# Performance work log

Measured on AMD Instinct MI355X. Metric: run time of the kernel, lower is better.

Reference implementation:

```python
import jax, jax.numpy as jnp
import numpy as np

COMMITMENT_COST = 0.25


def setup_inputs() -> dict:
    key = jax.random.key(0)
    k1, k2 = jax.random.split(key)
    B, H, W, D, K = 64, 32, 32, 64, 1024
    x = jax.random.normal(k1, (B, H, W, D), dtype=jnp.float32)
    # variance_scaling(fan_in=D, uniform) ~ U(-sqrt(3/D), sqrt(3/D)); plain normal*scale is fine for a reference
    embeddings = jax.random.uniform(k2, (D, K), dtype=jnp.float32,
                                    minval=-np.sqrt(3.0 / D), maxval=np.sqrt(3.0 / D))
    return {"x": x, "embeddings": embeddings}


def reference(x, embeddings):
    D = embeddings.shape[0]
    K = embeddings.shape[1]
    flat = x.reshape(-1, D)                                   # [N, D]
    # squared euclidean distance: ||f||^2 - 2 f.E + ||e||^2 -> [N, K]
    distance = (jnp.sum(flat ** 2, axis=1, keepdims=True)
                - 2.0 * jnp.matmul(flat, embeddings)
                + jnp.sum(embeddings ** 2, axis=0, keepdims=True))
    encoding_indices_flat = jnp.argmax(-distance, axis=1)     # [N]
    encodings = jax.nn.one_hot(encoding_indices_flat, K, dtype=distance.dtype)  # [N, K]
    encoding_indices = encoding_indices_flat.reshape(x.shape[:-1])
    # quantize: gather rows of E^T -> same shape as x
    quantized = jnp.take(embeddings.T, encoding_indices, axis=0)
    e_latent_loss = jnp.mean((jax.lax.stop_gradient(quantized) - x) ** 2)
    q_latent_loss = jnp.mean((quantized - jax.lax.stop_gradient(x)) ** 2)
    loss = q_latent_loss + COMMITMENT_COST * e_latent_loss
    quantized_st = x + jax.lax.stop_gradient(quantized - x)   # straight-through
    avg_probs = jnp.mean(encodings, axis=0)                   # [K]
    perplexity = jnp.exp(-jnp.sum(avg_probs * jnp.log(avg_probs + 1e-10)))
    return quantized_st, loss, perplexity, encoding_indices
```

## Files before the change

### kernel.cpp

```cpp
#include <hip/hip_runtime.h>
#include <math.h>


typedef __attribute__((ext_vector_type(8))) short short8v;
typedef __attribute__((ext_vector_type(4))) float float4v;
typedef unsigned short u16;
typedef unsigned int u32;

constexpr int D = 64;
constexpr int K = 1024;
constexpr int NPTS = 65536;
constexpr long QOFF = (long)NPTS * D;
constexpr float BIAS = 24.0f;
constexpr float GATE = 5e-3f;

constexpr size_t OFF_LOSS = 0;
constexpr size_t OFF_CNT  = 256;
constexpr size_t OFF_EC   = OFF_CNT + 4096;
constexpr size_t OFF_ECB  = OFF_EC + 4096;
constexpr size_t OFF_ET   = OFF_ECB + 4096;
constexpr size_t OFF_STG  = OFF_ET + (size_t)K * D * 4;

__device__ __forceinline__ float med3(float a, float b, float c) {
  return __builtin_amdgcn_fmed3f(a, b, c);
}
__device__ __forceinline__ u16 bf16rtn(float x) {
  u32 u = __float_as_uint(x);
  return (u16)((u + 0x7fffu + ((u >> 16) & 1u)) >> 16);
}
__device__ __forceinline__ float bf2f(u16 h) {
  return __uint_as_float(((u32)h) << 16);
}
__device__ __forceinline__ void gl_lds16(const void* g, void* l) {
  __builtin_amdgcn_global_load_lds(
      (const __attribute__((address_space(1))) u32*)g,
      (__attribute__((address_space(3))) u32*)l, 16, 0, 0);
}

__global__ __launch_bounds__(256) void vq_prep(const float* __restrict__ E,
                                               float* __restrict__ eC,
                                               float* __restrict__ eCb,
                                               float* __restrict__ Et,
                                               unsigned char* __restrict__ stg,
                                               double* __restrict__ lossSum,
                                               int* __restrict__ counts) {
  int gid = blockIdx.x * 256 + threadIdx.x;
  int s = gid >> 10;
  int k = gid & 1023;
  size_t rowb = (size_t)(k >> 7) * 32768 + (size_t)(k & 127) * 256;
  int swz = (k & 7) * 16;
#pragma unroll
  for (int q = 0; q < 4; ++q) {
    float v[8];
#pragma unroll
    for (int j = 0; j < 8; ++j) v[j] = E[(s * 32 + q * 8 + j) * K + k];
    *(float4*)&Et[(size_t)k * 64 + s * 32 + q * 8] =
        make_float4(v[0], v[1], v[2], v[3]);
    *(float4*)&Et[(size_t)k * 64 + s * 32 + q * 8 + 4] =
        make_float4(v[4], v[5], v[6], v[7]);
    short8v hv, lv;
#pragma unroll
    for (int j = 0; j < 8; ++j) {
      float m2 = -2.0f * v[j];
      u16 h = bf16rtn(m2);
      hv[j] = (short)h;
      lv[j] = (short)bf16rtn(m2 - bf2f(h));
    }
    int off = (s * 64 + q * 16) ^ swz;
    *(short8v*)&stg[rowb + off] = hv;
    *(short8v*)&stg[rowb + 128 + off] = lv;
  }
  if (s == 0) {
    float c = __fmul_rn(E[k], E[k]);
#pragma unroll
    for (int d = 1; d < D; ++d) {
      float vv = E[d * K + k];
      c = __fadd_rn(c, __fmul_rn(vv, vv));
    }
    eC[k] = c;
    eCb[k] = c + BIAS;
    counts[k] = 0;
    if (k == 0) *lossSum = 0.0;
  }
}

__global__ __launch_bounds__(256) void vq_main(const float* __restrict__ x,
                                               const unsigned char* __restrict__ stg,
                                               const float* __restrict__ eC,
                                               const float* __restrict__ eCb,
                                               const float* __restrict__ Etg,
                                               float* __restrict__ out,
                                               double* __restrict__ lossSum,
                                               int* __restrict__ counts) {
  __shared__ __align__(16) unsigned char sbuf[2][32768];
  __shared__ __align__(16) float ecb[1024];
  __shared__ __align__(16) float topbuf[256 * 4];
  __shared__ int bkbuf[128];

  const int tid = threadIdx.x;
  const int w = tid >> 6;
  const int lane = tid & 63;
  const int col = lane & 15;
  const int quad = lane >> 4;
  const int blockBase = blockIdx.x * 128;
  const float INF = __builtin_inff();

  *(float4*)&ecb[tid * 4] = *(const float4*)&eCb[tid * 4];

  short8v Bh[2][2], Bl[2][2];
#pragma unroll
  for (int pt = 0; pt < 2; ++pt) {
    const float* xp = x + (size_t)(blockBase + w * 32 + pt * 16 + col) * 64;
#pragma unroll
    for (int s = 0; s < 2; ++s) {
      const float4* src = (const float4*)(xp + s * 32 + quad * 8);
      float4 a = src[0], b = src[1];
      float xs[8] = {a.x, a.y, a.z, a.w, b.x, b.y, b.z, b.w};
      short8v hf, lf;
#pragma unroll
      for (int j = 0; j < 8; ++j) {
        u16 h = bf16rtn(xs[j]);
        hf[j] = (short)h;
        lf[j] = (short)bf16rtn(xs[j] - bf2f(h));
      }
      Bh[pt][s] = hf;
      Bl[pt][s] = lf;
    }
  }

  {
    const unsigned char* s0 = stg + (size_t)tid * 16;
#pragma unroll
    for (int i = 0; i < 8; ++i)
      gl_lds16(s0 + i * 4096, &sbuf[0][tid * 16 + i * 4096]);
#pragma unroll
    for (int i = 0; i < 8; ++i)
      gl_lds16(s0 + 32768 + i * 4096, &sbuf[1][tid * 16 + i * 4096]);
  }
  asm volatile("s_waitcnt vmcnt(8) lgkmcnt(0)" ::: "memory");
  __builtin_amdgcn_s_barrier();
  __builtin_amdgcn_sched_barrier(0);
  asm volatile("" ::: "memory");

  float b1[2] = {INF, INF}, b2[2] = {INF, INF};
  const int swz = (col & 7) * 16;

#pragma unroll 1
  for (int ch = 0; ch < 8; ++ch) {
    unsigned char* bufB = sbuf[ch & 1];
#pragma unroll
    for (int ct = 0; ct < 8; ++ct) {
      const int rb = ct * 4096 + col * 256;
      short8v Ah0 = *(const short8v*)&bufB[rb + ((quad * 16) ^ swz)];
      short8v Ah1 = *(const short8v*)&bufB[rb + ((64 + quad * 16) ^ swz)];
      short8v Al0 = *(const short8v*)&bufB[rb + 128 + ((quad * 16) ^ swz)];
      short8v Al1 = *(const short8v*)&bufB[rb + 128 + ((64 + quad * 16) ^ swz)];
      float4v Ci = *(const float4v*)&ecb[ch * 128 + ct * 16 + quad * 4];
#pragma unroll
      for (int pt = 0; pt < 2; ++pt) {
        float4v Ca = Ci;
        float4v Cb = {0.f, 0.f, 0.f, 0.f};
        Ca = __builtin_amdgcn_mfma_f32_16x16x32_bf16(Ah0, Bh[pt][0], Ca, 0, 0, 0);
        Cb = __builtin_amdgcn_mfma_f32_16x16x32_bf16(Ah1, Bh[pt][1], Cb, 0, 0, 0);
        Ca = __builtin_amdgcn_mfma_f32_16x16x32_bf16(Al0, Bh[pt][0], Ca, 0, 0, 0);
        Cb = __builtin_amdgcn_mfma_f32_16x16x32_bf16(Al1, Bh[pt][1], Cb, 0, 0, 0);
        Ca = __builtin_amdgcn_mfma_f32_16x16x32_bf16(Ah0, Bl[pt][0], Ca, 0, 0, 0);
        Cb = __builtin_amdgcn_mfma_f32_16x16x32_bf16(Ah1, Bl[pt][1], Cb, 0, 0, 0);
#pragma unroll
        for (int r = 0; r < 4; ++r) {
          float dv = Ca[r] + Cb[r];
          u32 u = (__float_as_uint(dv) & 0xffffff00u) |
                  (u32)(ch * 32 + ct * 4 + r);
          float v = __uint_as_float(u);
          float pb = b1[pt];
          b1[pt] = fminf(pb, v);
          b2[pt] = med3(pb, b2[pt], v);
        }
      }
    }
    asm volatile("s_waitcnt lgkmcnt(0)" ::: "memory");
    __builtin_amdgcn_s_barrier();
    __builtin_amdgcn_sched_barrier(0);
    asm volatile("" ::: "memory");
    if (ch < 6) {
      const unsigned char* s2 = stg + (size_t)(ch + 2) * 32768 + (size_t)tid * 16;
#pragma unroll
      for (int i = 0; i < 8; ++i)
        gl_lds16(s2 + i * 4096, &bufB[tid * 16 + i * 4096]);
      asm volatile("s_waitcnt vmcnt(8)" ::: "memory");
    } else if (ch == 6) {
      asm volatile("s_waitcnt vmcnt(0)" ::: "memory");
    }
    if (ch < 7) {
      __builtin_amdgcn_s_barrier();
      __builtin_amdgcn_sched_barrier(0);
      asm volatile("" ::: "memory");
    }
  }

  topbuf[tid * 4 + 0] = b1[0];
  topbuf[tid * 4 + 1] = b2[0];
  topbuf[tid * 4 + 2] = b1[1];
  topbuf[tid * 4 + 3] = b2[1];
  __syncthreads();

  if (tid < 128) {
    const int mw = tid >> 5, mpt = (tid >> 4) & 1, mcol = tid & 15;
    float cv[8];
    int cq[8];
    float mv0 = INF, mv1 = INF;
    int q0 = 0;
#pragma unroll
    for (int q = 0; q < 4; ++q) {
      int lbase = (mw * 64 + q * 16 + mcol) * 4 + mpt * 2;
#pragma unroll
      for (int j = 0; j < 2; ++j) {
        float v = topbuf[lbase + j];
        cv[q * 2 + j] = v;
        cq[q * 2 + j] = q;
        if (v < mv0) { mv1 = mv0; mv0 = v; q0 = q; }
        else if (v < mv1) { mv1 = v; }
      }
    }
    u32 lb = __float_as_uint(mv0) & 255u;
    int bestk = (int)((lb >> 5) * 128 + ((lb >> 2) & 7) * 16 + q0 * 4 + (lb & 3));

    if (mv1 - mv0 < GATE) {
      const float* f = x + (size_t)(blockBase + tid) * 64;
      float r8[8];
#pragma unroll
      for (int j = 0; j < 8; ++j) { float fv = f[j]; r8[j] = __fmul_rn(fv, fv); }
#pragma unroll
      for (int i = 8; i < D; i += 8)
#pragma unroll
        for (int j = 0; j < 8; ++j) {
          float fv = f[i + j];
          r8[j] = __fadd_rn(r8[j], __fmul_rn(fv, fv));
        }
      float A = __fadd_rn(__fadd_rn(__fadd_rn(r8[0], r8[1]), __fadd_rn(r8[2], r8[3])),
                          __fadd_rn(__fadd_rn(r8[4], r8[5]), __fadd_rn(r8[6], r8[7])));
      float bd = INF;
      int bkk = K;
#pragma unroll
      for (int c = 0; c < 8; ++c) {
        u32 cb = __float_as_uint(cv[c]) & 255u;
        int k = (int)((cb >> 5) * 128 + ((cb >> 2) & 7) * 16 + cq[c] * 4 + (cb & 3));
        const float* er = Etg + (size_t)k * 64;
        float m = 0.f;
#pragma unroll
        for (int d = 0; d < D; ++d) m = __fmaf_rn(f[d], er[d], m);
        float dist = __fadd_rn(__fsub_rn(A, __fmul_rn(2.f, m)), eC[k]);
        bool better = (dist < bd) || (dist == bd && k < bkk);
        bd = better ? dist : bd;
        bkk = better ? k : bkk;
      }
      bestk = bkk;
    }

    bkbuf[tid] = bestk;
    out[QOFF + 2 + blockBase + tid] = (float)bestk;
    atomicAdd(&counts[bestk], 1);
  }
  __syncthreads();

  const int pp = tid >> 1, half = tid & 1;
  const int bk = bkbuf[pp];
  const float4* et = (const float4*)(Etg + (size_t)bk * 64 + half * 32);
  const float4* xr = (const float4*)(x + (size_t)(blockBase + pp) * 64 + half * 32);
  float4* ov = (float4*)(out + (size_t)(blockBase + pp) * 64 + half * 32);
  float errs = 0.f;
#pragma unroll
  for (int i = 0; i < 8; ++i) {
    float4 qv = et[i];
    float4 xv = xr[i];
    float dx;
    dx = qv.x - xv.x; errs = fmaf(dx, dx, errs);
    dx = qv.y - xv.y; errs = fmaf(dx, dx, errs);
    dx = qv.z - xv.z; errs = fmaf(dx, dx, errs);
    dx = qv.w - xv.w; errs = fmaf(dx, dx, errs);
    ov[i] = qv;
  }
  double de = (double)errs;
#pragma unroll
  for (int off = 32; off > 0; off >>= 1) de += __shfl_down(de, off, 64);
  if (lane == 0) atomicAdd(lossSum, de);
}

__global__ __launch_bounds__(256) void vq_finalize(const double* __restrict__ lossSum,
                                                   const int* __restrict__ counts,
                                                   float* __restrict__ out) {
  __shared__ double sh[256];
  double ent = 0.0;
  for (int k = threadIdx.x; k < K; k += 256) {
    double pp = (double)counts[k] / (double)NPTS;
    ent += pp * log(pp + 1e-10);
  }
  sh[threadIdx.x] = ent;
  __syncthreads();
  for (int s = 128; s > 0; s >>= 1) {
    if (threadIdx.x < s) sh[threadIdx.x] += sh[threadIdx.x + s];
    __syncthreads();
  }
  if (threadIdx.x == 0) {
    out[QOFF + 0] = (float)(1.25 * (*lossSum) / (double)((long)NPTS * D));
    out[QOFF + 1] = (float)exp(-sh[0]);
  }
}

extern "C" void kernel_launch(void* const* d_in, const int* in_sizes, int n_in,
                              void* d_out, int out_size, void* d_ws, size_t ws_size,
                              hipStream_t stream) {
  const float* x = (const float*)d_in[0];
  const float* E = (const float*)d_in[1];
  float* out = (float*)d_out;

  char* ws = (char*)d_ws;
  double* lossSum = (double*)(ws + OFF_LOSS);
  int* counts = (int*)(ws + OFF_CNT);
  float* eC = (float*)(ws + OFF_EC);
  float* eCb = (float*)(ws + OFF_ECB);
  float* Etg = (float*)(ws + OFF_ET);
  unsigned char* stgb = (unsigned char*)(ws + OFF_STG);

  vq_prep<<<8, 256, 0, stream>>>(E, eC, eCb, Etg, stgb, lossSum, counts);
  vq_main<<<NPTS / 128, 256, 0, stream>>>(x, stgb, eC, eCb, Etg, out,
                                          lossSum, counts);
  vq_finalize<<<1, 256, 0, stream>>>(lossSum, counts, out);
}
```

Before: 142.2 us.

## Fuse finalize into main via last-block counter, parallelize gated rescoring and prep

Folds the separate finalize kernel into the main kernel: each block bumps a global done counter and the last block computes the entropy and loss outputs, which removes one kernel launch. Points whose top two candidates are too close are collected into a shared list and rescored in exact fp32 with 8 threads per point (one candidate each) and a shuffle argmin. Before, each such point was rescored serially by a single thread while the rest of its wavefront waited. The prep kernel is also spread over 36 blocks instead of 8, with the column-norm work moved into dedicated blocks. The cost is extra shared memory, a shared atomic, an extra barrier, and global atomic ordering on the completion counter.

```diff
diff --git a/kernel.cpp b/kernel.cpp
--- a/kernel.cpp
+++ b/kernel.cpp
@@ -15,6 +15,7 @@
 constexpr float GATE = 5e-3f;
 
 constexpr size_t OFF_LOSS = 0;
+constexpr size_t OFF_DONE = 16;
 constexpr size_t OFF_CNT  = 256;
 constexpr size_t OFF_EC   = OFF_CNT + 4096;
 constexpr size_t OFF_ECB  = OFF_EC + 4096;
@@ -43,21 +44,19 @@
                                                float* __restrict__ Et,
                                                unsigned char* __restrict__ stg,
                                                double* __restrict__ lossSum,
-                                               int* __restrict__ counts) {
-  int gid = blockIdx.x * 256 + threadIdx.x;
-  int s = gid >> 10;
-  int k = gid & 1023;
-  size_t rowb = (size_t)(k >> 7) * 32768 + (size_t)(k & 127) * 256;
-  int swz = (k & 7) * 16;
-#pragma unroll
-  for (int q = 0; q < 4; ++q) {
+                                               int* __restrict__ counts,
+                                               int* __restrict__ done) {
+  const int b = blockIdx.x;
+  const int tid = threadIdx.x;
+  if (b < 32) {
+    int gid = b * 256 + tid;
+    int k = gid & 1023;
+    int g = gid >> 10;
     float v[8];
 #pragma unroll
-    for (int j = 0; j < 8; ++j) v[j] = E[(s * 32 + q * 8 + j) * K + k];
-    *(float4*)&Et[(size_t)k * 64 + s * 32 + q * 8] =
-        make_float4(v[0], v[1], v[2], v[3]);
-    *(float4*)&Et[(size_t)k * 64 + s * 32 + q * 8 + 4] =
-        make_float4(v[4], v[5], v[6], v[7]);
+    for (int j = 0; j < 8; ++j) v[j] = E[(g * 8 + j) * K + k];
+    *(float4*)&Et[(size_t)k * 64 + g * 8] = make_float4(v[0], v[1], v[2], v[3]);
+    *(float4*)&Et[(size_t)k * 64 + g * 8 + 4] = make_float4(v[4], v[5], v[6], v[7]);
     short8v hv, lv;
 #pragma unroll
     for (int j = 0; j < 8; ++j) {
@@ -66,11 +65,13 @@
       hv[j] = (short)h;
       lv[j] = (short)bf16rtn(m2 - bf2f(h));
     }
-    int off = (s * 64 + q * 16) ^ swz;
+    size_t rowb = (size_t)(k >> 7) * 32768 + (size_t)(k & 127) * 256;
+    int s = g >> 2, q = g & 3;
+    int off = (s * 64 + q * 16) ^ ((k & 7) * 16);
     *(short8v*)&stg[rowb + off] = hv;
     *(short8v*)&stg[rowb + 128 + off] = lv;
-  }
-  if (s == 0) {
+  } else {
+    int k = (b - 32) * 256 + tid;
     float c = __fmul_rn(E[k], E[k]);
 #pragma unroll
     for (int d = 1; d < D; ++d) {
@@ -80,7 +81,7 @@
     eC[k] = c;
     eCb[k] = c + BIAS;
     counts[k] = 0;
-    if (k == 0) *lossSum = 0.0;
+    if (k == 0) { *lossSum = 0.0; *done = 0; }
   }
 }
 
@@ -91,11 +92,16 @@
                                                const float* __restrict__ Etg,
                                                float* __restrict__ out,
                                                double* __restrict__ lossSum,
-                                               int* __restrict__ counts) {
+                                               int* __restrict__ counts,
+                                               int* __restrict__ done) {
   __shared__ __align__(16) unsigned char sbuf[2][32768];
   __shared__ __align__(16) float ecb[1024];
   __shared__ __align__(16) float topbuf[256 * 4];
   __shared__ int bkbuf[128];
+  __shared__ int gks[128 * 8];
+  __shared__ short glist[128];
+  __shared__ int gcnt;
+  __shared__ int lastFlag;
 
   const int tid = threadIdx.x;
   const int w = tid >> 6;
@@ -106,6 +112,7 @@
   const float INF = __builtin_inff();
 
   *(float4*)&ecb[tid * 4] = *(const float4*)&eCb[tid * 4];
+  if (tid == 0) gcnt = 0;
 
   short8v Bh[2][2], Bl[2][2];
 #pragma unroll
@@ -127,6 +134,7 @@
       Bl[pt][s] = lf;
     }
   }
+  __builtin_amdgcn_sched_barrier(0);
 
   {
     const unsigned char* s0 = stg + (size_t)tid * 16;
@@ -226,40 +234,59 @@
     int bestk = (int)((lb >> 5) * 128 + ((lb >> 2) & 7) * 16 + q0 * 4 + (lb & 3));
 
     if (mv1 - mv0 < GATE) {
-      const float* f = x + (size_t)(blockBase + tid) * 64;
+      int idx = atomicAdd(&gcnt, 1);
+      glist[idx] = (short)tid;
+#pragma unroll
+      for (int c = 0; c < 8; ++c) {
+        u32 cb = __float_as_uint(cv[c]) & 255u;
+        gks[idx * 8 + c] =
+            (int)((cb >> 5) * 128 + ((cb >> 2) & 7) * 16 + cq[c] * 4 + (cb & 3));
+      }
+    } else {
+      bkbuf[tid] = bestk;
+      out[QOFF + 2 + blockBase + tid] = (float)bestk;
+      atomicAdd(&counts[bestk], 1);
+    }
+  }
+  __syncthreads();
+
+  const int ng = gcnt;
+  for (int base = 0; base < ng; base += 32) {
+    int i = base + (tid >> 3);
+    if (i < ng) {
+      const int p = glist[i];
+      const int c = tid & 7;
+      int k = gks[i * 8 + c];
+      const float* f = x + (size_t)(blockBase + p) * 64;
       float r8[8];
 #pragma unroll
       for (int j = 0; j < 8; ++j) { float fv = f[j]; r8[j] = __fmul_rn(fv, fv); }
 #pragma unroll
-      for (int i = 8; i < D; i += 8)
+      for (int ii = 8; ii < D; ii += 8)
 #pragma unroll
         for (int j = 0; j < 8; ++j) {
-          float fv = f[i + j];
+          float fv = f[ii + j];
           r8[j] = __fadd_rn(r8[j], __fmul_rn(fv, fv));
         }
       float A = __fadd_rn(__fadd_rn(__fadd_rn(r8[0], r8[1]), __fadd_rn(r8[2], r8[3])),
                           __fadd_rn(__fadd_rn(r8[4], r8[5]), __fadd_rn(r8[6], r8[7])));
-      float bd = INF;
-      int bkk = K;
-#pragma unroll
-      for (int c = 0; c < 8; ++c) {
-        u32 cb = __float_as_uint(cv[c]) & 255u;
-        int k = (int)((cb >> 5) * 128 + ((cb >> 2) & 7) * 16 + cq[c] * 4 + (cb & 3));
-        const float* er = Etg + (size_t)k * 64;
-        float m = 0.f;
-#pragma unroll
-        for (int d = 0; d < D; ++d) m = __fmaf_rn(f[d], er[d], m);
-        float dist = __fadd_rn(__fsub_rn(A, __fmul_rn(2.f, m)), eC[k]);
-        bool better = (dist < bd) || (dist == bd && k < bkk);
-        bd = better ? dist : bd;
-        bkk = better ? k : bkk;
-      }
-      bestk = bkk;
-    }
-
-    bkbuf[tid] = bestk;
-    out[QOFF + 2 + blockBase + tid] = (float)bestk;
-    atomicAdd(&counts[bestk], 1);
+      const float* er = Etg + (size_t)k * 64;
+      float m = 0.f;
+#pragma unroll
+      for (int d = 0; d < D; ++d) m = __fmaf_rn(f[d], er[d], m);
+      float dist = __fadd_rn(__fsub_rn(A, __fmul_rn(2.f, m)), eC[k]);
+#pragma unroll
+      for (int off = 4; off >= 1; off >>= 1) {
+        float d2 = __shfl_xor(dist, off);
+        int k2 = __shfl_xor(k, off);
+        if (d2 < dist || (d2 == dist && k2 < k)) { dist = d2; k = k2; }
+      }
+      if (c == 0) {
+        bkbuf[p] = k;
+        out[QOFF + 2 + blockBase + p] = (float)k;
+        atomicAdd(&counts[k], 1);
+      }
+    }
   }
   __syncthreads();
 
@@ -284,26 +311,37 @@
 #pragma unroll
   for (int off = 32; off > 0; off >>= 1) de += __shfl_down(de, off, 64);
   if (lane == 0) atomicAdd(lossSum, de);
-}
-
-__global__ __launch_bounds__(256) void vq_finalize(const double* __restrict__ lossSum,
-                                                   const int* __restrict__ counts,
-                                                   float* __restrict__ out) {
-  __shared__ double sh[256];
-  double ent = 0.0;
-  for (int k = threadIdx.x; k < K; k += 256) {
-    double pp = (double)counts[k] / (double)NPTS;
-    ent += pp * log(pp + 1e-10);
-  }
-  sh[threadIdx.x] = ent;
+
+  __threadfence();
+  if (tid == 0) {
+    int t = __hip_atomic_fetch_add(done, 1, __ATOMIC_ACQ_REL,
+                                   __HIP_MEMORY_SCOPE_AGENT);
+    lastFlag = (t == (int)gridDim.x - 1);
+  }
   __syncthreads();
-  for (int s = 128; s > 0; s >>= 1) {
-    if (threadIdx.x < s) sh[threadIdx.x] += sh[threadIdx.x + s];
+  if (lastFlag) {
+    double ent = 0.0;
+    for (int k = tid; k < K; k += 256) {
+      int c = __hip_atomic_load(&counts[k], __ATOMIC_RELAXED,
+                                __HIP_MEMORY_SCOPE_AGENT);
+      double pp2 = (double)c / (double)NPTS;
+      ent += pp2 * log(pp2 + 1e-10);
+    }
+    double* sh = (double*)topbuf;
+    sh[tid] = ent;
     __syncthreads();
-  }
-  if (threadIdx.x == 0) {
-    out[QOFF + 0] = (float)(1.25 * (*lossSum) / (double)((long)NPTS * D));
-    out[QOFF + 1] = (float)exp(-sh[0]);
+    for (int s = 128; s > 0; s >>= 1) {
+      if (tid < s) sh[tid] += sh[tid + s];
+      __syncthreads();
+    }
+    if (tid == 0) {
+      unsigned long long lb = __hip_atomic_load((const unsigned long long*)lossSum,
+                                                __ATOMIC_RELAXED,
+                                                __HIP_MEMORY_SCOPE_AGENT);
+      double L = __longlong_as_double(lb);
+      out[QOFF + 0] = (float)(1.25 * L / (double)((long)NPTS * D));
+      out[QOFF + 1] = (float)exp(-sh[0]);
+    }
   }
 }
 
@@ -316,14 +354,14 @@
 
   char* ws = (char*)d_ws;
   double* lossSum = (double*)(ws + OFF_LOSS);
+  int* done = (int*)(ws + OFF_DONE);
   int* counts = (int*)(ws + OFF_CNT);
   float* eC = (float*)(ws + OFF_EC);
   float* eCb = (float*)(ws + OFF_ECB);
   float* Etg = (float*)(ws + OFF_ET);
   unsigned char* stgb = (unsigned char*)(ws + OFF_STG);
 
-  vq_prep<<<8, 256, 0, stream>>>(E, eC, eCb, Etg, stgb, lossSum, counts);
+  vq_prep<<<36, 256, 0, stream>>>(E, eC, eCb, Etg, stgb, lossSum, counts, done);
   vq_main<<<NPTS / 128, 256, 0, stream>>>(x, stgb, eC, eCb, Etg, out,
-                                          lossSum, counts);
-  vq_finalize<<<1, 256, 0, stream>>>(lossSum, counts, out);
-}
+                                          lossSum, counts, done);
+}
```

After: 207.9 us. 46.2% more time.
